# Kernel optimization log

Hardware: AMD Instinct MI355X
Metric: run time of the kernel (lower is better)

Reference implementation:

```python
import jax, jax.numpy as jnp
import numpy as np

EPS_LN = 1e-5

def layer_norm(x, g, b):
    mu = x.mean(-1, keepdims=True)
    var = ((x - mu) ** 2).mean(-1, keepdims=True)
    return (x - mu) / jnp.sqrt(var + EPS_LN) * g + b

def spike(x):
    # MultiSpike: quantized spike activation, forward = clip(round(x), 0, 4)
    return jnp.clip(jnp.round(x), 0.0, 4.0)

def setup_inputs() -> dict:
    key = jax.random.key(0)
    ks = jax.random.split(key, 8)
    B, C, H, W = 16, 256, 56, 56
    hid = 128
    inp = {}
    inp['feature_map'] = jax.random.normal(ks[0], (B, C, H, W), jnp.float32)
    inp['audio_feature'] = jax.random.normal(ks[1], (B, 1, C), jnp.float32)
    # MINE params
    inp['w1'] = jax.random.normal(ks[2], (hid, 2 * C), jnp.float32) / np.sqrt(2 * C)
    inp['b1'] = jnp.zeros((hid,), jnp.float32)
    inp['g1'] = jnp.ones((hid,), jnp.float32)
    inp['beta1'] = jnp.zeros((hid,), jnp.float32)
    inp['w2'] = jax.random.normal(ks[3], (hid // 2, hid), jnp.float32) / np.sqrt(hid)
    inp['b2'] = jnp.zeros((hid // 2,), jnp.float32)
    inp['g2'] = jnp.ones((hid // 2,), jnp.float32)
    inp['beta2'] = jnp.zeros((hid // 2,), jnp.float32)
    inp['w3'] = jax.random.normal(ks[4], (1, hid // 2), jnp.float32) / np.sqrt(hid // 2)
    inp['b3'] = jnp.zeros((1,), jnp.float32)
    # MI params
    inp['pw'] = jax.random.normal(ks[5], (C, C), jnp.float32) / np.sqrt(C)
    inp['pb'] = jnp.zeros((C,), jnp.float32)
    inp['pg'] = jnp.ones((C,), jnp.float32)
    inp['pbeta'] = jnp.zeros((C,), jnp.float32)
    return inp

def reference(feature_map, audio_feature, w1, b1, g1, beta1, w2, b2, g2, beta2,
              w3, b3, pw, pb, pg, pbeta):
    B, C, H, W = feature_map.shape
    # visual tokens: [B*H*W, C]
    visual = feature_map.transpose(0, 2, 3, 1).reshape(B * H * W, C)
    # broadcast audio to every spatial position: [B*H*W, C]
    audio = jnp.broadcast_to(audio_feature[:, 0][:, None, None, :], (B, H, W, C)).reshape(B * H * W, C)
    # MINE MLP on joint features
    joint = jnp.concatenate([visual, audio], axis=1)            # [BHW, 2C]
    h = spike(layer_norm(joint @ w1.T + b1, g1, beta1))          # [BHW, 128]
    h = spike(layer_norm(h @ w2.T + b2, g2, beta2))              # [BHW, 64]
    mi = (h @ w3.T + b3)[:, 0]                                   # [BHW]
    mi_map = mi.reshape(B, 1, H * W)
    fm_flat = feature_map.reshape(B, C, H * W)
    # MI-weighted pooling: [B,1,C]
    x = jnp.einsum('bos,bcs->boc', mi_map, fm_flat)
    x = x @ pw.T + pb                                            # proj (dropout = eval identity)
    x = spike(layer_norm(x, pg, pbeta))                          # [B,1,C]
    fusion_map = jnp.einsum('bchw,bc->bchw', feature_map, x[:, 0])
    mi4 = mi_map.reshape(B, 1, H, W)
    mi4 = (mi4 - mi4.min()) / (mi4.max() - mi4.min() + 1e-6)     # global min-max norm
    return fusion_map, mi4
```

## Files before the change

### kernel.cpp

```cpp
#include <hip/hip_runtime.h>

#define HW 3136
#define NPOS 12845056

__device__ __forceinline__ unsigned fkey(float f) {
  unsigned u = __float_as_uint(f);
  return (u & 0x80000000u) ? ~u : (u | 0x80000000u);
}
__device__ __forceinline__ float funkey(unsigned u) {
  return __uint_as_float((u & 0x80000000u) ? (u & 0x7FFFFFFFu) : ~u);
}
__device__ __forceinline__ float spikef(float x) {
  return fminf(fmaxf(rintf(x), 0.0f), 4.0f);
}

__global__ __launch_bounds__(256) void prep_kernel(
    const float* __restrict__ audio, const float* __restrict__ w1,
    const float* __restrict__ b1, const float* __restrict__ w2,
    float* __restrict__ a_pre, float* __restrict__ w1t,
    float* __restrict__ w2t, float* __restrict__ pool,
    unsigned* __restrict__ mm)
{
  __shared__ float au[256];
  const int bx = blockIdx.x, t = threadIdx.x;
  if (bx < 128) {
    int idx = bx * 256 + t;
    int c = idx >> 7, j = idx & 127;
    w1t[idx] = w1[j * 512 + c];
  } else if (bx < 160) {
    int idx = (bx - 128) * 256 + t;
    int k = idx >> 6, j2 = idx & 63;
    w2t[idx] = w2[j2 * 128 + k];
  } else if (bx < 176) {
    int b = bx - 160;
    au[t] = audio[b * 256 + t];
    __syncthreads();
    int w = t >> 6, l = t & 63;
    float a0 = au[l], a1 = au[l + 64], a2 = au[l + 128], a3 = au[l + 192];
    for (int jj = 0; jj < 32; ++jj) {
      int j = w * 32 + jj;
      const float* row = w1 + j * 512 + 256;
      float s = row[l] * a0 + row[l + 64] * a1 + row[l + 128] * a2 + row[l + 192] * a3;
      #pragma unroll
      for (int off = 32; off; off >>= 1) s += __shfl_xor(s, off);
      if (l == 0) a_pre[b * 128 + j] = s + b1[j];
    }
  } else {
    for (int i = t; i < 4096; i += 256) pool[i] = 0.0f;
    if (t == 0) { mm[0] = 0xFFFFFFFFu; mm[1] = 0u; }
  }
}

__global__ __launch_bounds__(256, 3) void mlp_kernel(
    const float* __restrict__ fm, const float* __restrict__ w1t,
    const float* __restrict__ w2t, const float* __restrict__ b2,
    const float* __restrict__ w3, const float* __restrict__ b3,
    const float* __restrict__ g1, const float* __restrict__ be1,
    const float* __restrict__ g2, const float* __restrict__ be2,
    const float* __restrict__ a_pre, float* __restrict__ mi_out,
    float* __restrict__ pool, unsigned* __restrict__ mm)
{
  __shared__ __align__(16) float wbuf[8192];
  __shared__ float red[2][4][64];
  __shared__ float miL[64];

  const int b  = blockIdx.y;
  const int s0 = blockIdx.x * 64;
  const int t  = threadIdx.x;
  const int l  = t & 63;
  const int wv = __builtin_amdgcn_readfirstlane(t >> 6);

  const float* fmblk = fm + (size_t)b * 256 * HW + s0;
  const float* fp = fmblk + l;

  float acc[32];
  #pragma unroll
  for (int j = 0; j < 32; ++j) acc[j] = 0.f;

  #pragma unroll 1
  for (int ch = 0; ch < 4; ++ch) {
    if (ch) __syncthreads();
    {
      const float* src = w1t + ch * 8192 + wv * 256 + l * 4;
      float* dst = wbuf + wv * 256;
      #pragma unroll
      for (int i = 0; i < 8; ++i)
        __builtin_amdgcn_global_load_lds(
            (const __attribute__((address_space(1))) void*)(src + i * 1024),
            (__attribute__((address_space(3))) void*)(dst + i * 1024), 16, 0, 0);
    }
    __syncthreads();
    const float* wrow = wbuf + wv * 32;
    #pragma unroll 2
    for (int k = 0; k < 64; ++k) {
      float x = fp[(size_t)(ch * 64 + k) * HW];
      const float* wk = wrow + k * 128;
      float4 q0 = *(const float4*)(wk);
      float4 q1 = *(const float4*)(wk + 4);
      float4 q2 = *(const float4*)(wk + 8);
      float4 q3 = *(const float4*)(wk + 12);
      float4 q4 = *(const float4*)(wk + 16);
      float4 q5 = *(const float4*)(wk + 20);
      float4 q6 = *(const float4*)(wk + 24);
      float4 q7 = *(const float4*)(wk + 28);
      acc[ 0] = fmaf(x, q0.x, acc[ 0]); acc[ 1] = fmaf(x, q0.y, acc[ 1]);
      acc[ 2] = fmaf(x, q0.z, acc[ 2]); acc[ 3] = fmaf(x, q0.w, acc[ 3]);
      acc[ 4] = fmaf(x, q1.x, acc[ 4]); acc[ 5] = fmaf(x, q1.y, acc[ 5]);
      acc[ 6] = fmaf(x, q1.z, acc[ 6]); acc[ 7] = fmaf(x, q1.w, acc[ 7]);
      acc[ 8] = fmaf(x, q2.x, acc[ 8]); acc[ 9] = fmaf(x, q2.y, acc[ 9]);
      acc[10] = fmaf(x, q2.z, acc[10]); acc[11] = fmaf(x, q2.w, acc[11]);
      acc[12] = fmaf(x, q3.x, acc[12]); acc[13] = fmaf(x, q3.y, acc[13]);
      acc[14] = fmaf(x, q3.z, acc[14]); acc[15] = fmaf(x, q3.w, acc[15]);
      acc[16] = fmaf(x, q4.x, acc[16]); acc[17] = fmaf(x, q4.y, acc[17]);
      acc[18] = fmaf(x, q4.z, acc[18]); acc[19] = fmaf(x, q4.w, acc[19]);
      acc[20] = fmaf(x, q5.x, acc[20]); acc[21] = fmaf(x, q5.y, acc[21]);
      acc[22] = fmaf(x, q5.z, acc[22]); acc[23] = fmaf(x, q5.w, acc[23]);
      acc[24] = fmaf(x, q6.x, acc[24]); acc[25] = fmaf(x, q6.y, acc[25]);
      acc[26] = fmaf(x, q6.z, acc[26]); acc[27] = fmaf(x, q6.w, acc[27]);
      acc[28] = fmaf(x, q7.x, acc[28]); acc[29] = fmaf(x, q7.y, acc[29]);
      acc[30] = fmaf(x, q7.z, acc[30]); acc[31] = fmaf(x, q7.w, acc[31]);
    }
  }
  {
    const float4* ap = (const float4*)(a_pre + b * 128 + wv * 32);
    #pragma unroll
    for (int q = 0; q < 8; ++q) {
      float4 a4 = ap[q];
      acc[4*q+0] += a4.x; acc[4*q+1] += a4.y;
      acc[4*q+2] += a4.z; acc[4*q+3] += a4.w;
    }
  }

  float mu, inv;
  {
    float s = 0.f;
    #pragma unroll
    for (int j = 0; j < 32; ++j) s += acc[j];
    red[0][wv][l] = s;
    __syncthreads();
    mu = (red[0][0][l] + red[0][1][l] + red[0][2][l] + red[0][3][l]) * (1.0f/128.0f);
    float s2 = 0.f;
    #pragma unroll
    for (int j = 0; j < 32; ++j) { float d = acc[j] - mu; s2 = fmaf(d, d, s2); }
    red[1][wv][l] = s2;
    __syncthreads();
    float var = (red[1][0][l] + red[1][1][l] + red[1][2][l] + red[1][3][l]) * (1.0f/128.0f);
    inv = 1.0f / sqrtf(var + 1e-5f);
  }

  {
    const float* gp = g1  + wv * 32;
    const float* bp = be1 + wv * 32;
    #pragma unroll
    for (int j = 0; j < 32; ++j) {
      float h = spikef((acc[j] - mu) * inv * gp[j] + bp[j]);
      wbuf[(wv * 32 + j) * 64 + l] = h;
    }
  }
  __syncthreads();

  float a2[16];
  #pragma unroll
  for (int p = 0; p < 16; ++p) a2[p] = 0.f;
  {
    const float* hrow = wbuf + wv * 16;
    const float* w2p  = w2t + l;
    #pragma unroll 2
    for (int k2 = 0; k2 < 128; ++k2) {
      float w = w2p[k2 * 64];
      const float* hk = hrow + k2 * 64;
      float4 x0 = *(const float4*)(hk);
      float4 x1 = *(const float4*)(hk + 4);
      float4 x2 = *(const float4*)(hk + 8);
      float4 x3 = *(const float4*)(hk + 12);
      a2[ 0] = fmaf(x0.x, w, a2[ 0]); a2[ 1] = fmaf(x0.y, w, a2[ 1]);
      a2[ 2] = fmaf(x0.z, w, a2[ 2]); a2[ 3] = fmaf(x0.w, w, a2[ 3]);
      a2[ 4] = fmaf(x1.x, w, a2[ 4]); a2[ 5] = fmaf(x1.y, w, a2[ 5]);
      a2[ 6] = fmaf(x1.z, w, a2[ 6]); a2[ 7] = fmaf(x1.w, w, a2[ 7]);
      a2[ 8] = fmaf(x2.x, w, a2[ 8]); a2[ 9] = fmaf(x2.y, w, a2[ 9]);
      a2[10] = fmaf(x2.z, w, a2[10]); a2[11] = fmaf(x2.w, w, a2[11]);
      a2[12] = fmaf(x3.x, w, a2[12]); a2[13] = fmaf(x3.y, w, a2[13]);
      a2[14] = fmaf(x3.z, w, a2[14]); a2[15] = fmaf(x3.w, w, a2[15]);
    }
  }
  {
    const float b2l = b2[l];
    #pragma unroll
    for (int p = 0; p < 16; ++p) a2[p] += b2l;
  }

  float miv[16];
  {
    const float g2l = g2[l], be2l = be2[l], w3l = w3[l];
    const float b3v = b3[0];
    #pragma unroll
    for (int p = 0; p < 16; ++p) {
      float s = a2[p];
      #pragma unroll
      for (int off = 32; off; off >>= 1) s += __shfl_xor(s, off);
      float mu2 = s * (1.0f/64.0f);
      float d = a2[p] - mu2;
      float s2 = d * d;
      #pragma unroll
      for (int off = 32; off; off >>= 1) s2 += __shfl_xor(s2, off);
      float inv2 = 1.0f / sqrtf(s2 * (1.0f/64.0f) + 1e-5f);
      float sp = spikef(d * inv2 * g2l + be2l) * w3l;
      #pragma unroll
      for (int off = 32; off; off >>= 1) sp += __shfl_xor(sp, off);
      miv[p] = sp + b3v;
    }
  }

  {
    float m = miv[0];
    #pragma unroll
    for (int p = 1; p < 16; ++p) m = (l == p) ? miv[p] : m;
    if (l < 16) {
      mi_out[b * HW + s0 + wv * 16 + l] = m;
      miL[wv * 16 + l] = m;
    }
  }
  __syncthreads();

  if (wv == 0) {
    float v = miL[l];
    float mn = v, mx = v;
    #pragma unroll
    for (int off = 32; off; off >>= 1) {
      mn = fminf(mn, __shfl_xor(mn, off));
      mx = fmaxf(mx, __shfl_xor(mx, off));
    }
    if (l == 0) {
      unsigned kmn = fkey(mn), kmx = fkey(mx);
      volatile unsigned* vmm = (volatile unsigned*)mm;
      if (kmn < vmm[0]) atomicMin(&mm[0], kmn);
      if (kmx > vmm[1]) atomicMax(&mm[1], kmx);
    }
  }

  {
    const float mval = miL[l];
    const float* fp2 = fmblk + l + (size_t)(wv << 6) * HW;
    #pragma unroll 4
    for (int ci = 0; ci < 64; ++ci) {
      float v = fp2[(size_t)ci * HW] * mval;
      #pragma unroll
      for (int off = 32; off; off >>= 1) v += __shfl_xor(v, off);
      if (l == 0) atomicAdd(&pool[b * 256 + (wv << 6) + ci], v);
    }
  }
}

__global__ __launch_bounds__(256) void scale_kernel(
    const float* __restrict__ pool, const float* __restrict__ pw,
    const float* __restrict__ pb, const float* __restrict__ pg,
    const float* __restrict__ pbeta, float* __restrict__ scale,
    const unsigned* __restrict__ mm, float* __restrict__ gpar)
{
  __shared__ float pl[256];
  __shared__ float xsh[256];
  __shared__ float rs[4], rs2[4];
  int b = blockIdx.x, t = threadIdx.x;
  pl[t] = pool[b*256 + t];
  __syncthreads();
  int w = t >> 6, l = t & 63;
  float p0 = pl[l], p1 = pl[l+64], p2 = pl[l+128], p3 = pl[l+192];
  for (int jj = 0; jj < 64; ++jj) {
    int j = w*64 + jj;
    const float* row = pw + j*256;
    float s = row[l]*p0 + row[l+64]*p1 + row[l+128]*p2 + row[l+192]*p3;
    #pragma unroll
    for (int off = 32; off; off >>= 1) s += __shfl_xor(s, off);
    if (l == 0) xsh[j] = s;
  }
  __syncthreads();
  float x = xsh[t] + pb[t];
  float s = x;
  #pragma unroll
  for (int off = 32; off; off >>= 1) s += __shfl_xor(s, off);
  if (l == 0) rs[w] = s;
  __syncthreads();
  float mu = (rs[0]+rs[1]+rs[2]+rs[3]) * (1.0f/256.0f);
  float d = x - mu;
  float s2 = d*d;
  #pragma unroll
  for (int off = 32; off; off >>= 1) s2 += __shfl_xor(s2, off);
  if (l == 0) rs2[w] = s2;
  __syncthreads();
  float var = (rs2[0]+rs2[1]+rs2[2]+rs2[3]) * (1.0f/256.0f);
  float v = d / sqrtf(var + 1e-5f) * pg[t] + pbeta[t];
  scale[b*256 + t] = spikef(v);
  if (b == 0 && t == 0) {
    float mn = funkey(mm[0]), mx = funkey(mm[1]);
    gpar[0] = mn;
    gpar[1] = mx - mn + 1e-6f;
  }
}

__global__ __launch_bounds__(256) void fuse_kernel(
    const float4* __restrict__ fm4, const float* __restrict__ scale,
    const float4* __restrict__ mi4, const float* __restrict__ gpar,
    float4* __restrict__ out4, float4* __restrict__ mi4out)
{
  const int c = blockIdx.x, b = blockIdx.y, t = threadIdx.x;
  if (c < 256) {
    float s = scale[b * 256 + c];
    size_t base = ((size_t)b * 256 + c) * 784;
    #pragma unroll
    for (int i = 0; i < 3; ++i) {
      int idx = t + i * 256;
      float4 v = fm4[base + idx];
      out4[base + idx] = make_float4(v.x*s, v.y*s, v.z*s, v.w*s);
    }
    int idx = t + 768;
    if (idx < 784) {
      float4 v = fm4[base + idx];
      out4[base + idx] = make_float4(v.x*s, v.y*s, v.z*s, v.w*s);
    }
  } else {
    float gmin = gpar[0], den = gpar[1];
    size_t base = (size_t)b * 784;
    #pragma unroll
    for (int i = 0; i < 3; ++i) {
      int idx = t + i * 256;
      float4 v = mi4[base + idx];
      mi4out[base + idx] = make_float4((v.x-gmin)/den, (v.y-gmin)/den,
                                       (v.z-gmin)/den, (v.w-gmin)/den);
    }
    int idx = t + 768;
    if (idx < 784) {
      float4 v = mi4[base + idx];
      mi4out[base + idx] = make_float4((v.x-gmin)/den, (v.y-gmin)/den,
                                       (v.z-gmin)/den, (v.w-gmin)/den);
    }
  }
}

extern "C" void kernel_launch(void* const* d_in, const int* in_sizes, int n_in,
                              void* d_out, int out_size, void* d_ws, size_t ws_size,
                              hipStream_t stream)
{
  const float* fm    = (const float*)d_in[0];
  const float* audio = (const float*)d_in[1];
  const float* w1    = (const float*)d_in[2];
  const float* b1    = (const float*)d_in[3];
  const float* g1    = (const float*)d_in[4];
  const float* be1   = (const float*)d_in[5];
  const float* w2    = (const float*)d_in[6];
  const float* b2    = (const float*)d_in[7];
  const float* g2    = (const float*)d_in[8];
  const float* be2   = (const float*)d_in[9];
  const float* w3    = (const float*)d_in[10];
  const float* b3    = (const float*)d_in[11];
  const float* pw    = (const float*)d_in[12];
  const float* pb    = (const float*)d_in[13];
  const float* pg    = (const float*)d_in[14];
  const float* pbeta = (const float*)d_in[15];

  float* ws    = (float*)d_ws;
  float* a_pre = ws;
  float* pool  = ws + 2048;
  float* scale = ws + 6144;
  float* mi    = ws + 10240;
  float* w1t   = ws + 60416;
  float* w2t   = ws + 93184;
  unsigned* mm = (unsigned*)(ws + 101376);
  float* gpar  = ws + 101378;

  float* out    = (float*)d_out;
  float* mi4out = out + NPOS;

  prep_kernel<<<177, 256, 0, stream>>>(audio, w1, b1, w2, a_pre, w1t, w2t,
                                       pool, mm);
  mlp_kernel<<<dim3(49, 16), 256, 0, stream>>>(fm, w1t, w2t, b2, w3, b3,
                                               g1, be1, g2, be2,
                                               a_pre, mi, pool, mm);
  scale_kernel<<<16, 256, 0, stream>>>(pool, pw, pb, pg, pbeta, scale, mm, gpar);
  fuse_kernel<<<dim3(257, 16), 256, 0, stream>>>((const float4*)fm, scale,
                                                 (const float4*)mi, gpar,
                                                 (float4*)out, (float4*)mi4out);
}
```

Before: 327.5 us.

## Double-buffer feature and weight tiles in LDS and use 512-thread MLP blocks

The MLP kernel now runs 8 waves per block, each owning 16 hidden units instead of 32, and keeps fewer accumulators per thread. Both the feature-map tile and the w1 tile are staged into LDS through asynchronous global-to-LDS loads, double-buffered across 8 chunks of 32 channels, so the next chunk loads while the current one computes. The aim is more waves per CU and latency hiding for the strided feature loads that used to go straight from global memory. The cost is more LDS per block, a barrier per chunk, and a longer reduction across 8 waves for the layer norm.

```diff
diff --git a/kernel.cpp b/kernel.cpp
--- a/kernel.cpp
+++ b/kernel.cpp
@@ -51,7 +51,7 @@
   }
 }
 
-__global__ __launch_bounds__(256, 3) void mlp_kernel(
+__global__ __launch_bounds__(512, 6) void mlp_kernel(
     const float* __restrict__ fm, const float* __restrict__ w1t,
     const float* __restrict__ w2t, const float* __restrict__ b2,
     const float* __restrict__ w3, const float* __restrict__ b3,
@@ -60,8 +60,8 @@
     const float* __restrict__ a_pre, float* __restrict__ mi_out,
     float* __restrict__ pool, unsigned* __restrict__ mm)
 {
-  __shared__ __align__(16) float wbuf[8192];
-  __shared__ float red[2][4][64];
+  __shared__ __align__(16) float smem[12288];
+  __shared__ float red[16][64];
   __shared__ float miL[64];
 
   const int b  = blockIdx.y;
@@ -71,38 +71,47 @@
   const int wv = __builtin_amdgcn_readfirstlane(t >> 6);
 
   const float* fmblk = fm + (size_t)b * 256 * HW + s0;
-  const float* fp = fmblk + l;
-
-  float acc[32];
+  float* const h1f = smem;
+
+  auto stage = [&](int ch, int bd) {
+    {
+      const float* g = fmblk + (size_t)(ch * 32 + wv * 4 + (l >> 4)) * HW
+                       + (l & 15) * 4;
+      float* d = smem + bd * 2048 + wv * 256;
+      __builtin_amdgcn_global_load_lds(
+          (const __attribute__((address_space(1))) void*)g,
+          (__attribute__((address_space(3))) void*)d, 16, 0, 0);
+    }
+    #pragma unroll
+    for (int i = 0; i < 2; ++i) {
+      const float* g = w1t + (size_t)(ch * 32 + wv * 4 + i * 2 + (l >> 5)) * 128
+                       + (l & 31) * 4;
+      float* d = smem + 4096 + bd * 4096 + (wv * 4 + i * 2) * 128;
+      __builtin_amdgcn_global_load_lds(
+          (const __attribute__((address_space(1))) void*)g,
+          (__attribute__((address_space(3))) void*)d, 16, 0, 0);
+    }
+  };
+
+  float acc[16];
   #pragma unroll
-  for (int j = 0; j < 32; ++j) acc[j] = 0.f;
-
+  for (int j = 0; j < 16; ++j) acc[j] = 0.f;
+
+  stage(0, 0);
+  __syncthreads();
   #pragma unroll 1
-  for (int ch = 0; ch < 4; ++ch) {
-    if (ch) __syncthreads();
-    {
-      const float* src = w1t + ch * 8192 + wv * 256 + l * 4;
-      float* dst = wbuf + wv * 256;
-      #pragma unroll
-      for (int i = 0; i < 8; ++i)
-        __builtin_amdgcn_global_load_lds(
-            (const __attribute__((address_space(1))) void*)(src + i * 1024),
-            (__attribute__((address_space(3))) void*)(dst + i * 1024), 16, 0, 0);
-    }
-    __syncthreads();
-    const float* wrow = wbuf + wv * 32;
-    #pragma unroll 2
-    for (int k = 0; k < 64; ++k) {
-      float x = fp[(size_t)(ch * 64 + k) * HW];
-      const float* wk = wrow + k * 128;
+  for (int ch = 0; ch < 8; ++ch) {
+    if (ch < 7) stage(ch + 1, (ch + 1) & 1);
+    const float* Ab = smem + (ch & 1) * 2048;
+    const float* Bb = smem + 4096 + (ch & 1) * 4096 + wv * 16;
+    #pragma unroll 4
+    for (int k = 0; k < 32; ++k) {
+      float x = Ab[k * 64 + l];
+      const float* wk = Bb + k * 128;
       float4 q0 = *(const float4*)(wk);
       float4 q1 = *(const float4*)(wk + 4);
       float4 q2 = *(const float4*)(wk + 8);
       float4 q3 = *(const float4*)(wk + 12);
-      float4 q4 = *(const float4*)(wk + 16);
-      float4 q5 = *(const float4*)(wk + 20);
-      float4 q6 = *(const float4*)(wk + 24);
-      float4 q7 = *(const float4*)(wk + 28);
       acc[ 0] = fmaf(x, q0.x, acc[ 0]); acc[ 1] = fmaf(x, q0.y, acc[ 1]);
       acc[ 2] = fmaf(x, q0.z, acc[ 2]); acc[ 3] = fmaf(x, q0.w, acc[ 3]);
       acc[ 4] = fmaf(x, q1.x, acc[ 4]); acc[ 5] = fmaf(x, q1.y, acc[ 5]);
@@ -111,20 +120,13 @@
       acc[10] = fmaf(x, q2.z, acc[10]); acc[11] = fmaf(x, q2.w, acc[11]);
       acc[12] = fmaf(x, q3.x, acc[12]); acc[13] = fmaf(x, q3.y, acc[13]);
       acc[14] = fmaf(x, q3.z, acc[14]); acc[15] = fmaf(x, q3.w, acc[15]);
-      acc[16] = fmaf(x, q4.x, acc[16]); acc[17] = fmaf(x, q4.y, acc[17]);
-      acc[18] = fmaf(x, q4.z, acc[18]); acc[19] = fmaf(x, q4.w, acc[19]);
-      acc[20] = fmaf(x, q5.x, acc[20]); acc[21] = fmaf(x, q5.y, acc[21]);
-      acc[22] = fmaf(x, q5.z, acc[22]); acc[23] = fmaf(x, q5.w, acc[23]);
-      acc[24] = fmaf(x, q6.x, acc[24]); acc[25] = fmaf(x, q6.y, acc[25]);
-      acc[26] = fmaf(x, q6.z, acc[26]); acc[27] = fmaf(x, q6.w, acc[27]);
-      acc[28] = fmaf(x, q7.x, acc[28]); acc[29] = fmaf(x, q7.y, acc[29]);
-      acc[30] = fmaf(x, q7.z, acc[30]); acc[31] = fmaf(x, q7.w, acc[31]);
-    }
-  }
-  {
-    const float4* ap = (const float4*)(a_pre + b * 128 + wv * 32);
-    #pragma unroll
-    for (int q = 0; q < 8; ++q) {
+    }
+    __syncthreads();
+  }
+  {
+    const float4* ap = (const float4*)(a_pre + b * 128 + wv * 16);
+    #pragma unroll
+    for (int q = 0; q < 4; ++q) {
       float4 a4 = ap[q];
       acc[4*q+0] += a4.x; acc[4*q+1] += a4.y;
       acc[4*q+2] += a4.z; acc[4*q+3] += a4.w;
@@ -135,66 +137,65 @@
   {
     float s = 0.f;
     #pragma unroll
-    for (int j = 0; j < 32; ++j) s += acc[j];
-    red[0][wv][l] = s;
+    for (int j = 0; j < 16; ++j) s += acc[j];
+    red[wv][l] = s;
     __syncthreads();
-    mu = (red[0][0][l] + red[0][1][l] + red[0][2][l] + red[0][3][l]) * (1.0f/128.0f);
+    s = 0.f;
+    #pragma unroll
+    for (int q = 0; q < 8; ++q) s += red[q][l];
+    mu = s * (1.0f/128.0f);
     float s2 = 0.f;
     #pragma unroll
-    for (int j = 0; j < 32; ++j) { float d = acc[j] - mu; s2 = fmaf(d, d, s2); }
-    red[1][wv][l] = s2;
+    for (int j = 0; j < 16; ++j) { float d = acc[j] - mu; s2 = fmaf(d, d, s2); }
+    red[8 + wv][l] = s2;
     __syncthreads();
-    float var = (red[1][0][l] + red[1][1][l] + red[1][2][l] + red[1][3][l]) * (1.0f/128.0f);
-    inv = 1.0f / sqrtf(var + 1e-5f);
-  }
-
-  {
-    const float* gp = g1  + wv * 32;
-    const float* bp = be1 + wv * 32;
-    #pragma unroll
-    for (int j = 0; j < 32; ++j) {
+    s2 = 0.f;
+    #pragma unroll
+    for (int q = 0; q < 8; ++q) s2 += red[8 + q][l];
+    inv = 1.0f / sqrtf(s2 * (1.0f/128.0f) + 1e-5f);
+  }
+
+  {
+    const float* gp = g1  + wv * 16;
+    const float* bp = be1 + wv * 16;
+    #pragma unroll
+    for (int j = 0; j < 16; ++j) {
       float h = spikef((acc[j] - mu) * inv * gp[j] + bp[j]);
-      wbuf[(wv * 32 + j) * 64 + l] = h;
-    }
-  }
-  __syncthreads();
-
-  float a2[16];
+      h1f[(wv * 16 + j) * 64 + l] = h;
+    }
+  }
+  __syncthreads();
+
+  float a2[8];
   #pragma unroll
-  for (int p = 0; p < 16; ++p) a2[p] = 0.f;
-  {
-    const float* hrow = wbuf + wv * 16;
+  for (int p = 0; p < 8; ++p) a2[p] = 0.f;
+  {
+    const float* hrow = h1f + wv * 8;
     const float* w2p  = w2t + l;
     #pragma unroll 2
     for (int k2 = 0; k2 < 128; ++k2) {
-      float w = w2p[k2 * 64];
+      float wval = w2p[k2 * 64];
       const float* hk = hrow + k2 * 64;
       float4 x0 = *(const float4*)(hk);
       float4 x1 = *(const float4*)(hk + 4);
-      float4 x2 = *(const float4*)(hk + 8);
-      float4 x3 = *(const float4*)(hk + 12);
-      a2[ 0] = fmaf(x0.x, w, a2[ 0]); a2[ 1] = fmaf(x0.y, w, a2[ 1]);
-      a2[ 2] = fmaf(x0.z, w, a2[ 2]); a2[ 3] = fmaf(x0.w, w, a2[ 3]);
-      a2[ 4] = fmaf(x1.x, w, a2[ 4]); a2[ 5] = fmaf(x1.y, w, a2[ 5]);
-      a2[ 6] = fmaf(x1.z, w, a2[ 6]); a2[ 7] = fmaf(x1.w, w, a2[ 7]);
-      a2[ 8] = fmaf(x2.x, w, a2[ 8]); a2[ 9] = fmaf(x2.y, w, a2[ 9]);
-      a2[10] = fmaf(x2.z, w, a2[10]); a2[11] = fmaf(x2.w, w, a2[11]);
-      a2[12] = fmaf(x3.x, w, a2[12]); a2[13] = fmaf(x3.y, w, a2[13]);
-      a2[14] = fmaf(x3.z, w, a2[14]); a2[15] = fmaf(x3.w, w, a2[15]);
+      a2[0] = fmaf(x0.x, wval, a2[0]); a2[1] = fmaf(x0.y, wval, a2[1]);
+      a2[2] = fmaf(x0.z, wval, a2[2]); a2[3] = fmaf(x0.w, wval, a2[3]);
+      a2[4] = fmaf(x1.x, wval, a2[4]); a2[5] = fmaf(x1.y, wval, a2[5]);
+      a2[6] = fmaf(x1.z, wval, a2[6]); a2[7] = fmaf(x1.w, wval, a2[7]);
     }
   }
   {
     const float b2l = b2[l];
     #pragma unroll
-    for (int p = 0; p < 16; ++p) a2[p] += b2l;
-  }
-
-  float miv[16];
+    for (int p = 0; p < 8; ++p) a2[p] += b2l;
+  }
+
+  float miv[8];
   {
     const float g2l = g2[l], be2l = be2[l], w3l = w3[l];
     const float b3v = b3[0];
     #pragma unroll
-    for (int p = 0; p < 16; ++p) {
+    for (int p = 0; p < 8; ++p) {
       float s = a2[p];
       #pragma unroll
       for (int off = 32; off; off >>= 1) s += __shfl_xor(s, off);
@@ -214,10 +215,10 @@
   {
     float m = miv[0];
     #pragma unroll
-    for (int p = 1; p < 16; ++p) m = (l == p) ? miv[p] : m;
-    if (l < 16) {
-      mi_out[b * HW + s0 + wv * 16 + l] = m;
-      miL[wv * 16 + l] = m;
+    for (int p = 1; p < 8; ++p) m = (l == p) ? miv[p] : m;
+    if (l < 8) {
+      mi_out[b * HW + s0 + wv * 8 + l] = m;
+      miL[wv * 8 + l] = m;
     }
   }
   __syncthreads();
@@ -240,13 +241,13 @@
 
   {
     const float mval = miL[l];
-    const float* fp2 = fmblk + l + (size_t)(wv << 6) * HW;
+    const float* fp2 = fmblk + l + (size_t)(wv << 5) * HW;
     #pragma unroll 4
-    for (int ci = 0; ci < 64; ++ci) {
+    for (int ci = 0; ci < 32; ++ci) {
       float v = fp2[(size_t)ci * HW] * mval;
       #pragma unroll
       for (int off = 32; off; off >>= 1) v += __shfl_xor(v, off);
-      if (l == 0) atomicAdd(&pool[b * 256 + (wv << 6) + ci], v);
+      if (l == 0) atomicAdd(&pool[b * 256 + (wv << 5) + ci], v);
     }
   }
 }
@@ -372,7 +373,7 @@
 
   prep_kernel<<<177, 256, 0, stream>>>(audio, w1, b1, w2, a_pre, w1t, w2t,
                                        pool, mm);
-  mlp_kernel<<<dim3(49, 16), 256, 0, stream>>>(fm, w1t, w2t, b2, w3, b3,
+  mlp_kernel<<<dim3(49, 16), 512, 0, stream>>>(fm, w1t, w2t, b2, w3, b3,
                                                g1, be1, g2, be2,
                                                a_pre, mi, pool, mm);
   scale_kernel<<<16, 256, 0, stream>>>(pool, pw, pb, pg, pbeta, scale, mm, gpar);
```

Result: no change. 331.4 us (+1.2%).
